# Optimization experiments

Hardware: AMD Instinct MI355X
Metric: run time of the kernel (lower is better)

## Reference

```python
import jax, jax.numpy as jnp
import numpy as np

DIM = 1024
NUM_HEADS = 16
HEAD_DIM = DIM // NUM_HEADS


def setup_inputs() -> dict:
    key = jax.random.key(0)
    k1, k2, k3, k4, k5 = jax.random.split(key, 5)
    x = jax.random.normal(k1, (4, 4096, DIM), dtype=jnp.float32)
    # truncnormal002 init ~ std 0.02; plain normal*0.02 is a faithful stand-in for testing
    w_qkv = jax.random.normal(k2, (3 * DIM, DIM), dtype=jnp.float32) * 0.02
    b_qkv = jnp.zeros((3 * DIM,), dtype=jnp.float32)
    w_proj = jax.random.normal(k3, (DIM, DIM), dtype=jnp.float32) * 0.02
    b_proj = jnp.zeros((DIM,), dtype=jnp.float32)
    return {"x": x, "w_qkv": w_qkv, "b_qkv": b_qkv, "w_proj": w_proj, "b_proj": b_proj}


def reference(x, w_qkv, b_qkv, w_proj, b_proj):
    bs, seqlen, dim = x.shape
    # qkv projection (torch Linear: x @ W^T + b)
    qkv = x @ w_qkv.T + b_qkv  # [bs, seqlen, 3*dim]
    qkv = qkv.reshape(bs, seqlen, 3, NUM_HEADS, HEAD_DIM)
    qkv = jnp.transpose(qkv, (2, 0, 3, 1, 4))  # [3, bs, heads, seqlen, head_dim]
    q, k, v = qkv[0], qkv[1], qkv[2]
    q = jax.nn.softmax(q, axis=-1) * (HEAD_DIM ** -0.5)  # softmax over head_dim
    k = jax.nn.softmax(k, axis=-2)                        # softmax over seqlen
    # linear attention: kv state is [heads, head_dim, head_dim]
    kv = jnp.einsum('bhsd,bhse->bhde', k, v)  # k^T @ v
    out = jnp.einsum('bhsd,bhde->bhse', q, kv)  # q @ kv
    out = jnp.transpose(out, (0, 2, 1, 3)).reshape(bs, seqlen, dim)
    return out @ w_proj.T + b_proj
```

## Files before the change

### kernel.cpp

```cpp
#include <hip/hip_runtime.h>
#include <hip/hip_bf16.h>
#include <stdint.h>


#define DIM 1024
#define NH 16
#define HD 64
#define BSZ 4
#define SEQ 4096
#define MTOT (BSZ*SEQ)
#define NQKV (3*DIM)
#define QSCALE 0.125f
#define LOG2E 1.4426950408889634f

typedef __attribute__((ext_vector_type(8))) short bf16x8;
typedef __attribute__((ext_vector_type(4))) float f32x4;
typedef __attribute__((ext_vector_type(4))) float float4_t;
typedef __attribute__((ext_vector_type(4))) unsigned short ushort4_t;
typedef __attribute__((ext_vector_type(8))) unsigned short ushort8_t;

__device__ __forceinline__ unsigned short f2bf(float f) {
  uint32_t u = __builtin_bit_cast(uint32_t, f);
  u += 0x7fffu + ((u >> 16) & 1u);
  return (unsigned short)(u >> 16);
}
__device__ __forceinline__ float bf2f(unsigned short h) {
  uint32_t u = ((uint32_t)h) << 16;
  return __builtin_bit_cast(float, u);
}

#define GLD16(gp, lp) __builtin_amdgcn_global_load_lds( \
    (const __attribute__((address_space(1))) void*)(gp), \
    (__attribute__((address_space(3))) void*)(lp), 16, 0, 0)

__global__ __launch_bounds__(256) void cvt_kernel(
    const float* __restrict__ in, unsigned short* __restrict__ out, long n) {
  long i = ((long)blockIdx.x * 256 + threadIdx.x) * 8;
  if (i >= n) return;
  float4_t a = *(const float4_t*)(in + i);
  float4_t b = *(const float4_t*)(in + i + 4);
  ushort8_t r;
  r[0] = f2bf(a[0]); r[1] = f2bf(a[1]); r[2] = f2bf(a[2]); r[3] = f2bf(a[3]);
  r[4] = f2bf(b[0]); r[5] = f2bf(b[1]); r[6] = f2bf(b[2]); r[7] = f2bf(b[3]);
  *(ushort8_t*)(out + i) = r;
}

__global__ __launch_bounds__(256) void zero_f32(float* __restrict__ p) {
  int i = (blockIdx.x * 256 + threadIdx.x) * 4;
  *(float4_t*)(p + i) = (float4_t){0.f, 0.f, 0.f, 0.f};
}


#define LDA_(TB, MREP, KS) (*(const bf16x8*)(lds + (TB)*65536 + \
    (32*(MREP) + 16*wm + r4)*128 + ((((KS)*4 + g) ^ (r4 & 7))*16)))
#define LDB_(TB, NREP, KS) (*(const bf16x8*)(lds + (TB)*65536 + 32768 + \
    (wn*64 + (NREP)*16 + r4)*128 + ((((KS)*4 + g) ^ (r4 & 7))*16)))

#define STAGE(SB, ISB, H, KT_) do { \
    const unsigned short* _src = (ISB) ? B : A; \
    const int _rb = ((ISB) ? n0 : m0) + (H) * 128; \
    const unsigned short* _g0 = _src + (size_t)(_rb + srow) * Kdim + (KT_) * 64 + scol; \
    const unsigned short* _g1 = _src + (size_t)(_rb + 64 + srow) * Kdim + (KT_) * 64 + scol; \
    char* _l0 = lds + (SB) * 65536 + (ISB) * 32768 + (H) * 16384 + soff; \
    GLD16(_g0, _l0); \
    GLD16(_g1, _l0 + 8192); \
  } while (0)

#define MFMA_ __builtin_amdgcn_mfma_f32_16x16x32_bf16

#define PHASE(TB, P, LOADB, SB, SISB, SH, SKT, GATE) do { \
    if (LOADB) { \
      b00 = LDB_(TB,0,0); b01 = LDB_(TB,0,1); b10 = LDB_(TB,1,0); b11 = LDB_(TB,1,1); \
      b20 = LDB_(TB,2,0); b21 = LDB_(TB,2,1); b30 = LDB_(TB,3,0); b31 = LDB_(TB,3,1); \
    } \
    bf16x8 a00 = LDA_(TB,2*(P),0),   a01 = LDA_(TB,2*(P),1); \
    bf16x8 a10 = LDA_(TB,2*(P)+1,0), a11 = LDA_(TB,2*(P)+1,1); \
    STAGE(SB, SISB, SH, SKT); \
    __builtin_amdgcn_sched_barrier(0); \
    __builtin_amdgcn_s_barrier(); \
    asm volatile("s_waitcnt lgkmcnt(0)" ::: "memory"); \
    __builtin_amdgcn_sched_barrier(0); \
    __builtin_amdgcn_s_setprio(1); \
    acc[2*(P)][0]   = MFMA_(a00,b00,acc[2*(P)][0],0,0,0);   acc[2*(P)][0]   = MFMA_(a01,b01,acc[2*(P)][0],0,0,0); \
    acc[2*(P)][1]   = MFMA_(a00,b10,acc[2*(P)][1],0,0,0);   acc[2*(P)][1]   = MFMA_(a01,b11,acc[2*(P)][1],0,0,0); \
    acc[2*(P)][2]   = MFMA_(a00,b20,acc[2*(P)][2],0,0,0);   acc[2*(P)][2]   = MFMA_(a01,b21,acc[2*(P)][2],0,0,0); \
    acc[2*(P)][3]   = MFMA_(a00,b30,acc[2*(P)][3],0,0,0);   acc[2*(P)][3]   = MFMA_(a01,b31,acc[2*(P)][3],0,0,0); \
    acc[2*(P)+1][0] = MFMA_(a10,b00,acc[2*(P)+1][0],0,0,0); acc[2*(P)+1][0] = MFMA_(a11,b01,acc[2*(P)+1][0],0,0,0); \
    acc[2*(P)+1][1] = MFMA_(a10,b10,acc[2*(P)+1][1],0,0,0); acc[2*(P)+1][1] = MFMA_(a11,b11,acc[2*(P)+1][1],0,0,0); \
    acc[2*(P)+1][2] = MFMA_(a10,b20,acc[2*(P)+1][2],0,0,0); acc[2*(P)+1][2] = MFMA_(a11,b21,acc[2*(P)+1][2],0,0,0); \
    acc[2*(P)+1][3] = MFMA_(a10,b30,acc[2*(P)+1][3],0,0,0); acc[2*(P)+1][3] = MFMA_(a11,b31,acc[2*(P)+1][3],0,0,0); \
    __builtin_amdgcn_s_setprio(0); \
    __builtin_amdgcn_sched_barrier(0); \
    if (GATE) { asm volatile("s_waitcnt vmcnt(6)" ::: "memory"); } \
    __builtin_amdgcn_s_barrier(); \
    __builtin_amdgcn_sched_barrier(0); \
  } while (0)

template <int MODE>
__global__ __launch_bounds__(512, 2)
void gemm8p(const unsigned short* __restrict__ Aall,
            const unsigned short* __restrict__ Ball,
            const float* __restrict__ bias,
            unsigned short* __restrict__ Oq,
            unsigned short* __restrict__ Okt,
            unsigned short* __restrict__ Ovt,
            float* __restrict__ Of,
            int M, int Kdim)
{
  __shared__ __align__(16) char lds[131072];
  const int t = threadIdx.x, l = t & 63, wid = t >> 6;
  const int wm = wid >> 2, wn = wid & 3;
  const int r4 = l & 15, g = l >> 4;

  int bx, by;
  if (MODE == 0) {
    const int bid = blockIdx.y * gridDim.x + blockIdx.x;
    const int cpx = (gridDim.x * gridDim.y) >> 3;
    const int swz = (bid & 7) * cpx + (bid >> 3);
    bx = swz % gridDim.x;
    by = swz / gridDim.x;
  } else {
    bx = blockIdx.x; by = blockIdx.y;
  }
  const int m0 = bx * 256, n0 = by * 256;

  const unsigned short* A = Aall;
  const unsigned short* B = Ball;
  if (MODE == 1) {
    A += (size_t)blockIdx.z * M * Kdim;
    B += (size_t)blockIdx.z * DIM * Kdim;
  }

  const int srow = wid * 8 + (l >> 3);
  const int scol = ((l & 7) ^ (l >> 3)) * 8;
  const int soff = wid * 1024;

  f32x4 acc[8][4];
#pragma unroll
  for (int i = 0; i < 8; ++i)
#pragma unroll
    for (int j = 0; j < 4; ++j) acc[i][j] = (f32x4){0.f, 0.f, 0.f, 0.f};
  bf16x8 b00, b01, b10, b11, b20, b21, b30, b31;

  STAGE(0, 1, 0, 0); STAGE(0, 1, 1, 0); STAGE(0, 0, 0, 0); STAGE(0, 0, 1, 0);
  STAGE(1, 1, 0, 1); STAGE(1, 1, 1, 1); STAGE(1, 0, 0, 1);
  asm volatile("s_waitcnt vmcnt(6)" ::: "memory");
  __builtin_amdgcn_sched_barrier(0);
  __builtin_amdgcn_s_barrier();
  __builtin_amdgcn_sched_barrier(0);

  const int KT = Kdim >> 6;
  for (int it = 0; it < (KT >> 1); ++it) {
    const int t1 = 2 * it + 1;
    int t2 = 2 * it + 2; if (t2 >= KT) t2 -= KT;
    int t3 = 2 * it + 3; if (t3 >= KT) t3 -= KT;
    PHASE(0, 0, 1, 1, 0, 1, t1, 0);
    PHASE(0, 1, 0, 0, 1, 0, t2, 0);
    PHASE(0, 2, 0, 0, 1, 1, t2, 0);
    PHASE(0, 3, 0, 0, 0, 0, t2, 1);
    PHASE(1, 0, 1, 0, 0, 1, t2, 0);
    PHASE(1, 1, 0, 1, 1, 0, t3, 0);
    PHASE(1, 2, 0, 1, 1, 1, t3, 0);
    PHASE(1, 3, 0, 1, 0, 0, t3, 1);
  }

  if (MODE == 0) {
    const int region = n0 >> 10;
    float bv[4];
#pragma unroll
    for (int j = 0; j < 4; ++j) bv[j] = bias[n0 + wn * 64 + j * 16 + r4];
#pragma unroll
    for (int mi = 0; mi < 8; ++mi) {
      const int rowb = m0 + 32 * mi + 16 * wm + g * 4;
#pragma unroll
      for (int j = 0; j < 4; ++j) {
        const int col = n0 + wn * 64 + j * 16 + r4;
#pragma unroll
        for (int r = 0; r < 4; ++r) {
          const float val = acc[mi][j][r] + bv[j];
          const int rr = rowb + r;
          const unsigned short obf = f2bf(val);
          if (region == 0) {
            Oq[(size_t)rr * DIM + col] = obf;
          } else {
            const int n2 = col - region * DIM;
            const int b = rr >> 12, s = rr & 4095;
            const size_t bhd = (size_t)(b * NH + (n2 >> 6)) * HD + (n2 & 63);
            if (region == 1) Okt[bhd * SEQ + s] = obf;
            else             Ovt[bhd * SEQ + s] = obf;
          }
        }
      }
    }
  } else {
    float* Ob = Of + (size_t)blockIdx.z * M * DIM;
#pragma unroll
    for (int mi = 0; mi < 8; ++mi) {
      const int rowb = m0 + 32 * mi + 16 * wm + g * 4;
#pragma unroll
      for (int j = 0; j < 4; ++j) {
        const int col = n0 + wn * 64 + j * 16 + r4;
        const float bvj = bias[col];
#pragma unroll
        for (int r = 0; r < 4; ++r)
          Ob[(size_t)(rowb + r) * DIM + col] = acc[mi][j][r] + bvj;
      }
    }
  }
}

__global__ __launch_bounds__(256)
void colstats_rows(const unsigned short* __restrict__ Kt,
                   float* __restrict__ mcol, float* __restrict__ zcol)
{
  const int row = blockIdx.x * 4 + (threadIdx.x >> 6);
  const int lane = threadIdx.x & 63;
  const unsigned short* p = Kt + (size_t)row * SEQ + lane * 8;
  bf16x8 v[8];
#pragma unroll
  for (int c = 0; c < 8; ++c) v[c] = *(const bf16x8*)(p + c * 512);
  float mx = -1e30f;
#pragma unroll
  for (int c = 0; c < 8; ++c)
#pragma unroll
    for (int j = 0; j < 8; ++j) mx = fmaxf(mx, bf2f((unsigned short)v[c][j]));
#pragma unroll
  for (int off = 1; off < 64; off <<= 1) mx = fmaxf(mx, __shfl_xor(mx, off, 64));
  float s = 0.f;
#pragma unroll
  for (int c = 0; c < 8; ++c)
#pragma unroll
    for (int j = 0; j < 8; ++j) s += __expf(bf2f((unsigned short)v[c][j]) - mx);
#pragma unroll
  for (int off = 1; off < 64; off <<= 1) s += __shfl_xor(s, off, 64);
  if (lane == 0) { mcol[row] = mx; zcol[row] = s; }
}

__global__ __launch_bounds__(256)
void kv_mfma(const unsigned short* __restrict__ Kt, const unsigned short* __restrict__ Vt,
             const float* __restrict__ mcol, float* __restrict__ kvws)
{
  __shared__ __align__(16) unsigned short Ks[64 * 128];
  __shared__ __align__(16) unsigned short Vs[64 * 128];
  const int bh = blockIdx.x, ch = blockIdx.y;
  const int t = threadIdx.x, lane = t & 63, w = t >> 6;
  const int r = lane & 15, g = lane >> 4;

  const float mc = mcol[bh * 64 + 16 * w + r] * LOG2E;
  const size_t kbase = (size_t)bh * 64 * SEQ;

  f32x4 acc[4];
#pragma unroll
  for (int j = 0; j < 4; ++j) acc[j] = (f32x4){0.f, 0.f, 0.f, 0.f};

  int s0 = ch * 512;
  for (int st = 0; st < 4; ++st, s0 += 128) {
#pragma unroll
    for (int q = 0; q < 4; ++q) {
      const int d = 16 * w + 4 * q + g;
      const int gl = r ^ (d & 7);
      const size_t go = kbase + (size_t)d * SEQ + s0 + gl * 8;
      GLD16(Kt + go, Ks + (16 * w + 4 * q) * 128);
      GLD16(Vt + go, Vs + (16 * w + 4 * q) * 128);
    }
    __syncthreads();
#pragma unroll
    for (int ks = 0; ks < 4; ++ks) {
      const int coff = (((4 * ks + g) ^ (r & 7)) * 8);
      bf16x8 a = *(const bf16x8*)(Ks + (16 * w + r) * 128 + coff);
      bf16x8 ae;
#pragma unroll
      for (int j = 0; j < 8; ++j) {
        float f = bf2f((unsigned short)a[j]);
        float p = exp2f(f * LOG2E - mc);
        ae[j] = (short)f2bf(p);
      }
#pragma unroll
      for (int jt = 0; jt < 4; ++jt) {
        bf16x8 b = *(const bf16x8*)(Vs + (16 * jt + r) * 128 + coff);
        acc[jt] = __builtin_amdgcn_mfma_f32_16x16x32_bf16(ae, b, acc[jt], 0, 0, 0);
      }
    }
    __syncthreads();
  }
#pragma unroll
  for (int jt = 0; jt < 4; ++jt)
#pragma unroll
    for (int reg = 0; reg < 4; ++reg)
      atomicAdd(&kvws[((size_t)bh * 64 + 16 * w + g * 4 + reg) * 64 + 16 * jt + r],
                acc[jt][reg]);
}

__global__ __launch_bounds__(256)
void mbt_kernel(const float* __restrict__ kvws, const float* __restrict__ zcol,
                const float* __restrict__ wproj, unsigned short* __restrict__ MbT)
{
  __shared__ float kvl[64][65];
  const int b = blockIdx.x, h = blockIdx.y, nb = blockIdx.z;
  const int t = threadIdx.x;
  const int bh = b * NH + h;
  for (int u = t; u < 4096; u += 256) {
    int d = u >> 6, e = u & 63;
    float inv = QSCALE / zcol[bh * 64 + d];
    kvl[d][e] = kvws[((size_t)bh * 64 + d) * 64 + e] * inv;
  }
  __syncthreads();
  const int n = nb * 64 + (t >> 2);
  const int dg = (t & 3) * 16;
  const float* wrow = wproj + (size_t)n * DIM + h * HD;
  float out[16];
#pragma unroll
  for (int i = 0; i < 16; ++i) out[i] = 0.f;
  for (int e = 0; e < 64; e += 4) {
    float4_t w4 = *(const float4_t*)(wrow + e);
#pragma unroll
    for (int i = 0; i < 16; ++i)
      out[i] += w4[0] * kvl[dg + i][e] + w4[1] * kvl[dg + i][e + 1]
              + w4[2] * kvl[dg + i][e + 2] + w4[3] * kvl[dg + i][e + 3];
  }
  unsigned short* o = MbT + ((size_t)b * DIM + n) * DIM + h * HD + dg;
  ushort8_t o0, o1;
#pragma unroll
  for (int i = 0; i < 8; ++i) { o0[i] = f2bf(out[i]); o1[i] = f2bf(out[i + 8]); }
  *(ushort8_t*)(o) = o0;
  *(ushort8_t*)(o + 8) = o1;
}

__global__ __launch_bounds__(256)
void softmax_q(unsigned short* __restrict__ Q)
{
  const int t = threadIdx.x;
  const int lane = t & 63, wid = t >> 6;
  const size_t base = (((size_t)blockIdx.x * 4 + wid) * 256) + (size_t)lane * 4;
  ushort4_t q4 = *(const ushort4_t*)(Q + base);
  float x0 = bf2f(q4[0]), x1 = bf2f(q4[1]), x2 = bf2f(q4[2]), x3 = bf2f(q4[3]);
  float mx = fmaxf(fmaxf(x0, x1), fmaxf(x2, x3));
  for (int off = 1; off < 16; off <<= 1) mx = fmaxf(mx, __shfl_xor(mx, off, 16));
  float e0 = __expf(x0 - mx), e1 = __expf(x1 - mx);
  float e2 = __expf(x2 - mx), e3 = __expf(x3 - mx);
  float s = e0 + e1 + e2 + e3;
  for (int off = 1; off < 16; off <<= 1) s += __shfl_xor(s, off, 16);
  const float inv = 1.f / s;
  ushort4_t rr;
  rr[0] = f2bf(e0 * inv); rr[1] = f2bf(e1 * inv);
  rr[2] = f2bf(e2 * inv); rr[3] = f2bf(e3 * inv);
  *(ushort4_t*)(Q + base) = rr;
}

extern "C" void kernel_launch(void* const* d_in, const int* in_sizes, int n_in,
                              void* d_out, int out_size, void* d_ws, size_t ws_size,
                              hipStream_t stream)
{
  const float* x      = (const float*)d_in[0];
  const float* w_qkv  = (const float*)d_in[1];
  const float* b_qkv  = (const float*)d_in[2];
  const float* w_proj = (const float*)d_in[3];
  const float* b_proj = (const float*)d_in[4];
  float* out = (float*)d_out;

  char* ws = (char*)d_ws;
  size_t off = 0;
  auto alloc = [&](size_t bytes) -> void* {
    void* p = ws + off;
    off += (bytes + 255) & ~(size_t)255;
    return p;
  };
  unsigned short* xb   = (unsigned short*)alloc(2ull * MTOT * DIM);
  unsigned short* wqb  = (unsigned short*)alloc(2ull * NQKV * DIM);
  unsigned short* Qb   = (unsigned short*)alloc(2ull * MTOT * DIM);
  unsigned short* Ktb  = (unsigned short*)alloc(2ull * MTOT * DIM);
  unsigned short* Vtb  = (unsigned short*)alloc(2ull * MTOT * DIM);
  float* mcol  = (float*)alloc(4ull * 4096);
  float* zcol  = (float*)alloc(4ull * 4096);
  float* kvws  = (float*)alloc(4ull * 64 * 64 * 64);
  unsigned short* MbT = (unsigned short*)alloc(2ull * BSZ * DIM * DIM);
  if (off > ws_size) return;

  cvt_kernel<<<8192, 256, 0, stream>>>(x, xb, (long)MTOT * DIM);
  cvt_kernel<<<1536, 256, 0, stream>>>(w_qkv, wqb, (long)NQKV * DIM);

  gemm8p<0><<<dim3(64, 12), 512, 0, stream>>>(xb, wqb, b_qkv, Qb, Ktb, Vtb,
                                              nullptr, MTOT, DIM);

  colstats_rows<<<1024, 256, 0, stream>>>(Ktb, mcol, zcol);

  zero_f32<<<256, 256, 0, stream>>>(kvws);
  kv_mfma<<<dim3(64, 8), 256, 0, stream>>>(Ktb, Vtb, mcol, kvws);
  mbt_kernel<<<dim3(4, 16, 16), 256, 0, stream>>>(kvws, zcol, w_proj, MbT);

  softmax_q<<<16384, 256, 0, stream>>>(Qb);

  gemm8p<1><<<dim3(16, 4, 4), 512, 0, stream>>>(Qb, MbT, b_proj,
                                                nullptr, nullptr, nullptr, out,
                                                SEQ, DIM);
}
```

Before: 403.4 us.

## Write QKV GEMM output row-major and transpose K/V in a separate kernel

The QKV GEMM epilogue now writes a contiguous row-major [M, 3*DIM] bf16 buffer instead of scattering K and V into transposed layouts with strided 2-byte stores. A new transpose_kv kernel builds the K^T and V^T buffers with vectorized loads and stores, reusing the x buffer for V^T. softmax_q and the projection GEMM read Q in place through a leading-dimension argument. The aim is to replace the uncoalesced scattered epilogue stores, at the cost of an extra kernel launch plus a read and rewrite of the K/V data.

```diff
diff --git a/kernel.cpp b/kernel.cpp
--- a/kernel.cpp
+++ b/kernel.cpp
@@ -58,9 +58,10 @@
 
 #define STAGE(SB, ISB, H, KT_) do { \
     const unsigned short* _src = (ISB) ? B : A; \
+    const int _ld = (ISB) ? ldb : lda; \
     const int _rb = ((ISB) ? n0 : m0) + (H) * 128; \
-    const unsigned short* _g0 = _src + (size_t)(_rb + srow) * Kdim + (KT_) * 64 + scol; \
-    const unsigned short* _g1 = _src + (size_t)(_rb + 64 + srow) * Kdim + (KT_) * 64 + scol; \
+    const unsigned short* _g0 = _src + (size_t)(_rb + srow) * _ld + (KT_) * 64 + scol; \
+    const unsigned short* _g1 = _src + (size_t)(_rb + 64 + srow) * _ld + (KT_) * 64 + scol; \
     char* _l0 = lds + (SB) * 65536 + (ISB) * 32768 + (H) * 16384 + soff; \
     GLD16(_g0, _l0); \
     GLD16(_g1, _l0 + 8192); \
@@ -101,11 +102,9 @@
 void gemm8p(const unsigned short* __restrict__ Aall,
             const unsigned short* __restrict__ Ball,
             const float* __restrict__ bias,
-            unsigned short* __restrict__ Oq,
-            unsigned short* __restrict__ Okt,
-            unsigned short* __restrict__ Ovt,
+            unsigned short* __restrict__ Obf,
             float* __restrict__ Of,
-            int M, int Kdim)
+            int M, int Kdim, int lda, int ldb, int ldo)
 {
   __shared__ __align__(16) char lds[131072];
   const int t = threadIdx.x, l = t & 63, wid = t >> 6;
@@ -127,8 +126,8 @@
   const unsigned short* A = Aall;
   const unsigned short* B = Ball;
   if (MODE == 1) {
-    A += (size_t)blockIdx.z * M * Kdim;
-    B += (size_t)blockIdx.z * DIM * Kdim;
+    A += (size_t)blockIdx.z * M * lda;
+    B += (size_t)blockIdx.z * DIM * ldb;
   }
 
   const int srow = wid * 8 + (l >> 3);
@@ -165,7 +164,6 @@
   }
 
   if (MODE == 0) {
-    const int region = n0 >> 10;
     float bv[4];
 #pragma unroll
     for (int j = 0; j < 4; ++j) bv[j] = bias[n0 + wn * 64 + j * 16 + r4];
@@ -173,40 +171,62 @@
     for (int mi = 0; mi < 8; ++mi) {
       const int rowb = m0 + 32 * mi + 16 * wm + g * 4;
 #pragma unroll
-      for (int j = 0; j < 4; ++j) {
-        const int col = n0 + wn * 64 + j * 16 + r4;
-#pragma unroll
-        for (int r = 0; r < 4; ++r) {
-          const float val = acc[mi][j][r] + bv[j];
-          const int rr = rowb + r;
-          const unsigned short obf = f2bf(val);
-          if (region == 0) {
-            Oq[(size_t)rr * DIM + col] = obf;
-          } else {
-            const int n2 = col - region * DIM;
-            const int b = rr >> 12, s = rr & 4095;
-            const size_t bhd = (size_t)(b * NH + (n2 >> 6)) * HD + (n2 & 63);
-            if (region == 1) Okt[bhd * SEQ + s] = obf;
-            else             Ovt[bhd * SEQ + s] = obf;
-          }
-        }
+      for (int r = 0; r < 4; ++r) {
+        unsigned short* orow = Obf + (size_t)(rowb + r) * ldo + n0 + wn * 64 + r4;
+#pragma unroll
+        for (int j = 0; j < 4; ++j)
+          orow[j * 16] = f2bf(acc[mi][j][r] + bv[j]);
       }
     }
   } else {
-    float* Ob = Of + (size_t)blockIdx.z * M * DIM;
+    float* Ob = Of + (size_t)blockIdx.z * M * ldo;
 #pragma unroll
     for (int mi = 0; mi < 8; ++mi) {
       const int rowb = m0 + 32 * mi + 16 * wm + g * 4;
 #pragma unroll
-      for (int j = 0; j < 4; ++j) {
-        const int col = n0 + wn * 64 + j * 16 + r4;
-        const float bvj = bias[col];
-#pragma unroll
-        for (int r = 0; r < 4; ++r)
-          Ob[(size_t)(rowb + r) * DIM + col] = acc[mi][j][r] + bvj;
+      for (int r = 0; r < 4; ++r) {
+        float* orow = Ob + (size_t)(rowb + r) * ldo + n0 + wn * 64 + r4;
+#pragma unroll
+        for (int j = 0; j < 4; ++j)
+          orow[j * 16] = acc[mi][j][r] + bias[n0 + wn * 64 + j * 16 + r4];
       }
     }
   }
+}
+
+__global__ __launch_bounds__(256)
+void transpose_kv(const unsigned short* __restrict__ QKVb,
+                  unsigned short* __restrict__ Kt,
+                  unsigned short* __restrict__ Vt)
+{
+  const int bh = blockIdx.x;
+  const int S0 = blockIdx.y * 128;
+  unsigned short* dst = (blockIdx.z == 0) ? Kt : Vt;
+  const int c0 = (1 + blockIdx.z) * 1024 + (bh & 15) * 64;
+  const int t = threadIdx.x, l = t & 63, w = t >> 6;
+  const int d0 = (l & 15) * 4;
+  const int sg = (l >> 4) * 8;
+  const size_t R0 = (size_t)(bh >> 4) * SEQ + S0 + w * 32 + sg;
+
+  uint32_t lo[8], hi[8];
+#pragma unroll
+  for (int j = 0; j < 8; ++j) {
+    uint2 v = *(const uint2*)(QKVb + (R0 + j) * NQKV + c0 + d0);
+    lo[j] = v.x; hi[j] = v.y;
+  }
+  ushort8_t o0, o1, o2, o3;
+#pragma unroll
+  for (int j = 0; j < 8; ++j) {
+    o0[j] = (unsigned short)(lo[j] & 0xffff);
+    o1[j] = (unsigned short)(lo[j] >> 16);
+    o2[j] = (unsigned short)(hi[j] & 0xffff);
+    o3[j] = (unsigned short)(hi[j] >> 16);
+  }
+  const size_t obase = ((size_t)bh * 64 + d0) * SEQ + S0 + w * 32 + sg;
+  *(ushort8_t*)(dst + obase)           = o0;
+  *(ushort8_t*)(dst + obase + SEQ)     = o1;
+  *(ushort8_t*)(dst + obase + 2 * SEQ) = o2;
+  *(ushort8_t*)(dst + obase + 3 * SEQ) = o3;
 }
 
 __global__ __launch_bounds__(256)
@@ -327,12 +347,12 @@
 }
 
 __global__ __launch_bounds__(256)
-void softmax_q(unsigned short* __restrict__ Q)
+void softmax_q(unsigned short* __restrict__ QKVb)
 {
   const int t = threadIdx.x;
   const int lane = t & 63, wid = t >> 6;
-  const size_t base = (((size_t)blockIdx.x * 4 + wid) * 256) + (size_t)lane * 4;
-  ushort4_t q4 = *(const ushort4_t*)(Q + base);
+  const size_t base = (size_t)blockIdx.x * NQKV + wid * 256 + lane * 4;
+  ushort4_t q4 = *(const ushort4_t*)(QKVb + base);
   float x0 = bf2f(q4[0]), x1 = bf2f(q4[1]), x2 = bf2f(q4[2]), x3 = bf2f(q4[3]);
   float mx = fmaxf(fmaxf(x0, x1), fmaxf(x2, x3));
   for (int off = 1; off < 16; off <<= 1) mx = fmaxf(mx, __shfl_xor(mx, off, 16));
@@ -344,7 +364,7 @@
   ushort4_t rr;
   rr[0] = f2bf(e0 * inv); rr[1] = f2bf(e1 * inv);
   rr[2] = f2bf(e2 * inv); rr[3] = f2bf(e3 * inv);
-  *(ushort4_t*)(Q + base) = rr;
+  *(ushort4_t*)(QKVb + base) = rr;
 }
 
 extern "C" void kernel_launch(void* const* d_in, const int* in_sizes, int n_in,
@@ -367,20 +387,22 @@
   };
   unsigned short* xb   = (unsigned short*)alloc(2ull * MTOT * DIM);
   unsigned short* wqb  = (unsigned short*)alloc(2ull * NQKV * DIM);
-  unsigned short* Qb   = (unsigned short*)alloc(2ull * MTOT * DIM);
+  unsigned short* QKVb = (unsigned short*)alloc(2ull * MTOT * NQKV);
   unsigned short* Ktb  = (unsigned short*)alloc(2ull * MTOT * DIM);
-  unsigned short* Vtb  = (unsigned short*)alloc(2ull * MTOT * DIM);
   float* mcol  = (float*)alloc(4ull * 4096);
   float* zcol  = (float*)alloc(4ull * 4096);
   float* kvws  = (float*)alloc(4ull * 64 * 64 * 64);
   unsigned short* MbT = (unsigned short*)alloc(2ull * BSZ * DIM * DIM);
+  unsigned short* Vtb = xb;
   if (off > ws_size) return;
 
   cvt_kernel<<<8192, 256, 0, stream>>>(x, xb, (long)MTOT * DIM);
   cvt_kernel<<<1536, 256, 0, stream>>>(w_qkv, wqb, (long)NQKV * DIM);
 
-  gemm8p<0><<<dim3(64, 12), 512, 0, stream>>>(xb, wqb, b_qkv, Qb, Ktb, Vtb,
-                                              nullptr, MTOT, DIM);
+  gemm8p<0><<<dim3(64, 12), 512, 0, stream>>>(xb, wqb, b_qkv, QKVb, nullptr,
+                                              MTOT, DIM, DIM, DIM, NQKV);
+
+  transpose_kv<<<dim3(64, 32, 2), 256, 0, stream>>>(QKVb, Ktb, Vtb);
 
   colstats_rows<<<1024, 256, 0, stream>>>(Ktb, mcol, zcol);
 
@@ -388,9 +410,8 @@
   kv_mfma<<<dim3(64, 8), 256, 0, stream>>>(Ktb, Vtb, mcol, kvws);
   mbt_kernel<<<dim3(4, 16, 16), 256, 0, stream>>>(kvws, zcol, w_proj, MbT);
 
-  softmax_q<<<16384, 256, 0, stream>>>(Qb);
-
-  gemm8p<1><<<dim3(16, 4, 4), 512, 0, stream>>>(Qb, MbT, b_proj,
-                                                nullptr, nullptr, nullptr, out,
-                                                SEQ, DIM);
-}
+  softmax_q<<<16384, 256, 0, stream>>>(QKVb);
+
+  gemm8p<1><<<dim3(16, 4, 4), 512, 0, stream>>>(QKVb, MbT, b_proj, nullptr, out,
+                                                SEQ, DIM, NQKV, DIM, DIM);
+}
```

New measurement: 369.0 us. 8.5% less time.
